# Kernel optimization log

Hardware: AMD Instinct MI355X
Metric: run time of the kernel (lower is better)

The kernel has to match this reference:

```python
import jax, jax.numpy as jnp
import numpy as np

B, N1, N2, D, O = 4, 256, 256, 64, 64
TEMP = 1.0
BN_EPS = 1e-5


def setup_inputs() -> dict:
    key = jax.random.key(0)
    ks = jax.random.split(key, 24)
    s = lambda n: 1.0 / np.sqrt(n)
    inp = {
        'x1': jax.random.normal(ks[0], (B, N1, D), jnp.float32),
        'x2': jax.random.normal(ks[1], (B, N2, D), jnp.float32),
        'W_t1': jax.random.normal(ks[2], (D, D), jnp.float32) * s(D),
        'b_t1': jnp.zeros((D,), jnp.float32),
        'W_t2': jax.random.normal(ks[3], (D, D), jnp.float32) * s(D),
        'b_t2': jnp.zeros((D,), jnp.float32),
        'W_att': jax.random.normal(ks[4], (D, O), jnp.float32) * s(D),
        'b_att': jnp.zeros((O,), jnp.float32),
        'W_attM': jax.random.normal(ks[5], (D, O), jnp.float32) * s(D),
        'b_attM': jnp.zeros((O,), jnp.float32),
        'w11': jax.random.normal(ks[6], (O, 1), jnp.float32) * s(O),
        'w22': jax.random.normal(ks[7], (O, 1), jnp.float32) * s(O),
        'w12': jax.random.normal(ks[8], (O, 1), jnp.float32) * s(O),
        'wM': jax.random.normal(ks[9], (O, 1), jnp.float32) * s(O),
        'W_pa': jax.random.normal(ks[10], (D, O), jnp.float32) * s(D),
        'b_pa': jnp.zeros((O,), jnp.float32),
        'W_po': jax.random.normal(ks[11], (D, O), jnp.float32) * s(D),
        'b_po': jnp.zeros((O,), jnp.float32),
        'W_paM': jax.random.normal(ks[12], (D, O), jnp.float32) * s(D),
        'b_paM': jnp.zeros((O,), jnp.float32),
        'W_poM': jax.random.normal(ks[13], (D, O), jnp.float32) * s(D),
        'b_poM': jnp.zeros((O,), jnp.float32),
        'gamma': jnp.ones((O,), jnp.float32),
        'beta': jnp.zeros((O,), jnp.float32),
    }
    return inp


def _forward(x1, x2, W_t1, b_t1, W_t2, b_t2, W_att, b_att, W_attM, b_attM,
             w11, w22, w12, wM, W_pa, b_pa, W_po, b_po, W_paM, b_paM,
             W_poM, b_poM, gamma, beta):
    n1 = x1.shape[1]
    h1 = x1 @ W_t1 + b_t1                      # (B,n1,D)
    h2 = x2 @ W_t2 + b_t2                      # (B,n2,D)
    x = jnp.concatenate([h1, h2], axis=1)      # (B,N,D)
    master = jnp.mean(x, axis=1, keepdims=True)  # (B,1,D)

    # --- type-blocked attention map ---
    pair = x[:, :, None, :] * x[:, None, :, :]          # (B,N,N,D)
    e = jnp.tanh(pair @ W_att + b_att)                   # (B,N,N,O)
    s11 = jnp.einsum('bijd,d->bij', e[:, :n1, :n1], w11[:, 0])
    s12 = jnp.einsum('bijd,d->bij', e[:, :n1, n1:], w12[:, 0])
    s21 = jnp.einsum('bijd,d->bij', e[:, n1:, :n1], w12[:, 0])
    s22 = jnp.einsum('bijd,d->bij', e[:, n1:, n1:], w22[:, 0])
    top = jnp.concatenate([s11, s12], axis=2)
    bot = jnp.concatenate([s21, s22], axis=2)
    scores = jnp.concatenate([top, bot], axis=1)         # (B,N,N)
    att = jax.nn.softmax(scores / TEMP, axis=2)          # softmax over source nodes (torch dim=-2 of (B,N,N,1))

    # --- master update ---
    m = jnp.tanh((x * master) @ W_attM + b_attM)         # (B,N,O)
    aM = jax.nn.softmax((m @ wM) / TEMP, axis=1)         # (B,N,1)
    agg_m = jnp.einsum('bn,bnd->bd', aM[:, :, 0], x)[:, None, :]  # (B,1,D)
    master_new = (agg_m @ W_paM + b_paM) + (master @ W_poM + b_poM)

    # --- node projection + BN(eval) + SELU ---
    agg = jnp.einsum('bij,bjd->bid', att, x)             # (B,N,D)
    y = (agg @ W_pa + b_pa) + (x @ W_po + b_po)          # (B,N,O)
    y = y / jnp.sqrt(1.0 + BN_EPS) * gamma + beta        # BN eval: mean=0, var=1
    y = jax.nn.selu(y)
    return y[:, :n1], y[:, n1:], master_new


def reference(x1, x2, W_t1, b_t1, W_t2, b_t2, W_att, b_att, W_attM, b_attM,
              w11, w22, w12, wM, W_pa, b_pa, W_po, b_po, W_paM, b_paM,
              W_poM, b_poM, gamma, beta):
    return _forward(x1, x2, W_t1, b_t1, W_t2, b_t2, W_att, b_att, W_attM,
                    b_attM, w11, w22, w12, wM, W_pa, b_pa, W_po, b_po,
                    W_paM, b_paM, W_poM, b_poM, gamma, beta)
```

## Files before the change

### kernel.cpp

```cpp
#include <hip/hip_runtime.h>

#define BB 4
#define NN 512
#define NH 256
#define DD 64

typedef __attribute__((ext_vector_type(8))) short bf16x8;
typedef __attribute__((ext_vector_type(16))) float f32x16;
union BF8 { bf16x8 v; unsigned int u[4]; };
union BF8Q { bf16x8 v; uint4 q; };

__device__ __forceinline__ float wred_sum(float v) {
  v += __shfl_xor(v, 32);
  v += __shfl_xor(v, 16);
  v += __shfl_xor(v, 8);
  v += __shfl_xor(v, 4);
  v += __shfl_xor(v, 2);
  v += __shfl_xor(v, 1);
  return v;
}

__device__ __forceinline__ float wred_max(float v) {
  v = fmaxf(v, __shfl_xor(v, 32));
  v = fmaxf(v, __shfl_xor(v, 16));
  v = fmaxf(v, __shfl_xor(v, 8));
  v = fmaxf(v, __shfl_xor(v, 4));
  v = fmaxf(v, __shfl_xor(v, 2));
  v = fmaxf(v, __shfl_xor(v, 1));
  return v;
}

__device__ __forceinline__ unsigned int cvtpk_bf16(float lo, float hi) {
  unsigned int r;
  asm("v_cvt_pk_bf16_f32 %0, %1, %2" : "=v"(r) : "v"(lo), "v"(hi));
  return r;
}

__device__ __forceinline__ float fast_exp2(float x) {
  float r;
  asm("v_exp_f32 %0, %1" : "=v"(r) : "v"(x));
  return r;
}

__device__ __forceinline__ float fast_tanh(float t) {
  t = fminf(15.f, fmaxf(-15.f, t));
  float z = __expf(2.f * t);
  return 1.f - 2.f * __builtin_amdgcn_rcpf(z + 1.f);
}

__device__ __forceinline__ float bflo(unsigned int u) { return __uint_as_float(u << 16); }
__device__ __forceinline__ float bfhi(unsigned int u) { return __uint_as_float(u & 0xffff0000u); }

__global__ __launch_bounds__(256)
void k1_build_x(const float* __restrict__ x1, const float* __restrict__ x2,
                const float* __restrict__ W_t1, const float* __restrict__ b_t1,
                const float* __restrict__ W_t2, const float* __restrict__ b_t2,
                unsigned int* __restrict__ XbfG) {
  const int tid = threadIdx.x;
  const int lane = tid & 63;
  const int rq = tid >> 6;
  const int r = blockIdx.x * 4 + rq;
  const int b = r >> 9;
  const int n = r & 511;
  const float* src; const float* W; const float* bias;
  if (n < NH) { src = x1 + (b * NH + n) * DD;        W = W_t1; bias = b_t1; }
  else        { src = x2 + (b * NH + (n - NH)) * DD; W = W_t2; bias = b_t2; }
  const float4* s4 = reinterpret_cast<const float4*>(src);
  float t0 = 0.f, t1 = 0.f, t2 = 0.f, t3 = 0.f;
#pragma unroll
  for (int c = 0; c < 16; ++c) {
    const float4 v = s4[c];
    t0 = fmaf(v.x, W[(4 * c + 0) * DD + lane], t0);
    t1 = fmaf(v.y, W[(4 * c + 1) * DD + lane], t1);
    t2 = fmaf(v.z, W[(4 * c + 2) * DD + lane], t2);
    t3 = fmaf(v.w, W[(4 * c + 3) * DD + lane], t3);
  }
  const float yv = ((t0 + t1) + (t2 + t3)) + bias[lane];
  const float nb = __shfl_down(yv, 1);
  if ((lane & 1) == 0) XbfG[r * 32 + (lane >> 1)] = cvtpk_bf16(yv, nb);
}

__global__ __launch_bounds__(512, 1)
void k_sc(const unsigned int* __restrict__ Xbf,
          const float* __restrict__ W_att, const float* __restrict__ b_att,
          const float* __restrict__ w11, const float* __restrict__ w22,
          const float* __restrict__ w12,
          float* __restrict__ scG) {
  const int b = blockIdx.y;
  const int bx = blockIdx.x;
  const int tid = threadIdx.x;
  const int lane = tid & 63;
  const int w = tid >> 6;
  const int l31 = lane & 31;
  const int half = lane >> 5;

  __shared__ __align__(16) float tblB[64];
  __shared__ __align__(16) unsigned int A2L[4][32];

  const unsigned int* __restrict__ Xb = Xbf + b * NN * 32;
  float* __restrict__ scb = scG + b * NN * NN;
  const float K2E = 2.8853900817779268f;

  if (tid < 64) {
    const int ot = tid >> 5, hf = (tid >> 4) & 1, r = tid & 15;
    const int o = ot * 32 + (r & 3) + 8 * (r >> 2) + 4 * hf;
    tblB[tid] = K2E * b_att[o];
  }
  if (tid >= 64 && tid < 320) {
    const int tt = tid - 64;
    const int comb = tt >> 6;
    const int idx = tt & 63;
    if (idx < 32) {
      const int ot = (idx >> 4) & 1, kg = (idx >> 3) & 1, hf = (idx >> 2) & 1, pp = idx & 3;
      const int it_ = comb >> 1, jt_ = comb & 1;
      const float* wsl = it_ ? (jt_ ? w22 : w12) : (jt_ ? w12 : w11);
      const int e0 = 2 * pp, e1 = 2 * pp + 1;
      const int o0 = ot * 32 + kg * 16 + (e0 & 3) + 8 * (e0 >> 2) + 4 * hf;
      const int o1 = ot * 32 + kg * 16 + (e1 & 3) + 8 * (e1 >> 2) + 4 * hf;
      A2L[comb][idx] = cvtpk_bf16(wsl[o0], wsl[o1]);
    }
  }

  BF8 Wp[2][4];
#pragma unroll
  for (int ot = 0; ot < 2; ++ot)
#pragma unroll
    for (int kt = 0; kt < 4; ++kt) {
      const int o = ot * 32 + l31;
#pragma unroll
      for (int pp = 0; pp < 4; ++pp) {
        const int d0 = kt * 16 + half * 8 + 2 * pp;
        Wp[ot][kt].u[pp] = cvtpk_bf16(W_att[d0 * DD + o], W_att[(d0 + 1) * DD + o]);
      }
    }

  __syncthreads();

  const int cminA = bx >> 4;
  const int n32A = 16 - cminA;
  const int rB = 510 - 2 * bx;
  const int cminB = (255 - bx) >> 4;
  const int njobs = 2 * (n32A + (16 - cminB));

#pragma unroll 1
  for (int jb = w; jb < njobs; jb += 8) {
    int row, c32;
    if (jb < 2 * n32A) { row = 2 * bx + (jb & 1); c32 = cminA + (jb >> 1); }
    else { const int tp = jb - 2 * n32A; row = rB + (tp & 1); c32 = cminB + (tp >> 1); }
    const int j0 = c32 * 32;
    const int comb = ((row >= NH) ? 2 : 0) | ((j0 >= NH) ? 1 : 0);

    BF8 Bi[4];
#pragma unroll
    for (int kt = 0; kt < 4; ++kt) {
      const uint4 xi = *reinterpret_cast<const uint4*>(Xb + row * 32 + kt * 8 + half * 4);
      const uint4 xj = *reinterpret_cast<const uint4*>(Xb + (j0 + l31) * 32 + kt * 8 + half * 4);
      Bi[kt].u[0] = cvtpk_bf16(bflo(xi.x) * bflo(xj.x), bfhi(xi.x) * bfhi(xj.x));
      Bi[kt].u[1] = cvtpk_bf16(bflo(xi.y) * bflo(xj.y), bfhi(xi.y) * bfhi(xj.y));
      Bi[kt].u[2] = cvtpk_bf16(bflo(xi.z) * bflo(xj.z), bfhi(xi.z) * bfhi(xj.z));
      Bi[kt].u[3] = cvtpk_bf16(bflo(xi.w) * bflo(xj.w), bfhi(xi.w) * bfhi(xj.w));
    }

    f32x16 C0 = {}, C1 = {};
#pragma unroll
    for (int kt = 0; kt < 4; ++kt) {
      C0 = __builtin_amdgcn_mfma_f32_32x32x16_bf16(Wp[0][kt].v, Bi[kt].v, C0, 0, 0, 0);
      C1 = __builtin_amdgcn_mfma_f32_32x32x16_bf16(Wp[1][kt].v, Bi[kt].v, C1, 0, 0, 0);
    }

    f32x16 D2 = {};
    const int base = half * 16;
#pragma unroll
    for (int ot = 0; ot < 2; ++ot) {
      float tv[16];
#pragma unroll
      for (int r = 0; r < 16; ++r) {
        const float Cr = (ot == 0) ? C0[r] : C1[r];
        const float arg = fmaf(Cr, K2E, tblB[ot * 32 + base + r]);
        const float e = fast_exp2(arg);
        tv[r] = fmaf(-2.f, __builtin_amdgcn_rcpf(e + 1.f), 1.f);
      }
      BF8 B2a, B2b;
#pragma unroll
      for (int pp = 0; pp < 4; ++pp) {
        B2a.u[pp] = cvtpk_bf16(tv[2 * pp], tv[2 * pp + 1]);
        B2b.u[pp] = cvtpk_bf16(tv[8 + 2 * pp], tv[9 + 2 * pp]);
      }
      BF8Q A2a, A2b;
      A2a.q = *reinterpret_cast<const uint4*>(&A2L[comb][ot * 16 + half * 4]);
      A2b.q = *reinterpret_cast<const uint4*>(&A2L[comb][ot * 16 + 8 + half * 4]);
      D2 = __builtin_amdgcn_mfma_f32_32x32x16_bf16(A2a.v, B2a.v, D2, 0, 0, 0);
      D2 = __builtin_amdgcn_mfma_f32_32x32x16_bf16(A2b.v, B2b.v, D2, 0, 0, 0);
    }
    const float pout = D2[0];
    if (lane < 32) {
      const int j = j0 + l31;
      if (j >= row) {
        scb[row * NN + j] = pout;
        if (j > row) scb[j * NN + row] = pout;
      }
    }
  }
}

__global__ __launch_bounds__(1024, 4)
void k_rest(const unsigned int* __restrict__ Xbf, const float* __restrict__ scG,
            const float* __restrict__ W_attM, const float* __restrict__ b_attM,
            const float* __restrict__ wM,
            const float* __restrict__ W_pa, const float* __restrict__ b_pa,
            const float* __restrict__ W_po, const float* __restrict__ b_po,
            const float* __restrict__ gamma, const float* __restrict__ beta,
            float* __restrict__ master, float* __restrict__ logits,
            float* __restrict__ out) {
  const int b = blockIdx.y;
  const int i0 = blockIdx.x * 8;
  const int tid = threadIdx.x;
  const int lane = tid & 63;
  const int w = tid >> 6;
  const int l31 = lane & 31;
  const int half = lane >> 5;

  __shared__ __align__(16) unsigned int XbfL[NN * 32];
  __shared__ __align__(16) float scL[8 * NN];
  __shared__ __align__(16) float red2[16][DD];
  __shared__ __align__(16) float aggP[32][DD];
  __shared__ __align__(16) float aggL[8][DD];
  __shared__ __align__(16) float mastL[64];

  const unsigned int* __restrict__ Xb = Xbf + b * NN * 32;

  {
#pragma unroll
    for (int k = 0; k < 4; ++k)
      reinterpret_cast<uint4*>(XbfL)[tid + k * 1024] =
          reinterpret_cast<const uint4*>(Xb)[tid + k * 1024];
  }
  {
    const int r8 = tid >> 7;
    const int c = (tid & 127) * 4;
    *reinterpret_cast<float4*>(&scL[r8 * NN + c]) =
        *reinterpret_cast<const float4*>(&scG[(b * NN + i0 + r8) * NN + c]);
  }
  __syncthreads();

  {
    float se = 0.f, so = 0.f;
    for (int r = w * 32; r < w * 32 + 32; ++r) {
      const unsigned int u = XbfL[r * 32 + l31];
      se += bflo(u); so += bfhi(u);
    }
    if (half == 0) {
      float2 pr; pr.x = se; pr.y = so;
      *reinterpret_cast<float2*>(&red2[w][l31 * 2]) = pr;
    }
  }
  __syncthreads();
  if (w == 0) {
    float s = 0.f;
#pragma unroll
    for (int k = 0; k < 16; ++k) s += red2[k][lane];
    s *= (1.f / 512.f);
    mastL[lane] = s;
    if (blockIdx.x == 0) master[b * DD + lane] = s;
  }

  const int row = w & 7, part = w >> 3;
  const int irow = i0 + row;
  float v[8];
#pragma unroll
  for (int k = 0; k < 8; ++k) v[k] = scL[row * NN + lane + 64 * k];
  __syncthreads();
  float mx = fmaxf(fmaxf(fmaxf(v[0], v[1]), fmaxf(v[2], v[3])),
                   fmaxf(fmaxf(v[4], v[5]), fmaxf(v[6], v[7])));
  mx = wred_max(mx);
  float ssum = 0.f;
#pragma unroll
  for (int k = 0; k < 8; ++k) { v[k] = __expf(v[k] - mx); ssum += v[k]; }
  ssum = wred_sum(ssum);
  const float inv = __builtin_amdgcn_rcpf(ssum);
#pragma unroll
  for (int k = 0; k < 4; ++k) {
    const int kk = part * 4 + k;
    scL[row * NN + lane + 64 * kk] = v[kk] * inv;
  }

  {
    float ae = 0.f, ao = 0.f;
    const int jb = part * 256 + half * 128;
#pragma unroll 4
    for (int it = 0; it < 32; ++it) {
      const int j = jb + it * 4;
      const float4 at = *reinterpret_cast<const float4*>(&scL[row * NN + j]);
      const unsigned int u0 = XbfL[(j + 0) * 32 + l31];
      const unsigned int u1 = XbfL[(j + 1) * 32 + l31];
      const unsigned int u2 = XbfL[(j + 2) * 32 + l31];
      const unsigned int u3 = XbfL[(j + 3) * 32 + l31];
      ae = fmaf(at.x, bflo(u0), ae); ao = fmaf(at.x, bfhi(u0), ao);
      ae = fmaf(at.y, bflo(u1), ae); ao = fmaf(at.y, bfhi(u1), ao);
      ae = fmaf(at.z, bflo(u2), ae); ao = fmaf(at.z, bfhi(u2), ao);
      ae = fmaf(at.w, bflo(u3), ae); ao = fmaf(at.w, bfhi(u3), ao);
    }
    float2 pr; pr.x = ae; pr.y = ao;
    *reinterpret_cast<float2*>(&aggP[row * 4 + part * 2 + half][l31 * 2]) = pr;
  }
  __syncthreads();

  uint4 xr[8];
#pragma unroll
  for (int s = 0; s < 8; ++s)
    xr[s] = *reinterpret_cast<const uint4*>(&XbfL[irow * 32 + s * 4]);

  if (part == 0) {
    const float aggv = aggP[row * 4 + 0][lane] + aggP[row * 4 + 1][lane] +
                       aggP[row * 4 + 2][lane] + aggP[row * 4 + 3][lane];
    aggL[row][lane] = aggv;
    float y = b_pa[lane] + b_po[lane];
#pragma unroll
    for (int s = 0; s < 8; ++s) {
      const float xd[8] = {bflo(xr[s].x), bfhi(xr[s].x), bflo(xr[s].y), bfhi(xr[s].y),
                           bflo(xr[s].z), bfhi(xr[s].z), bflo(xr[s].w), bfhi(xr[s].w)};
      const float4 agA = *reinterpret_cast<const float4*>(&aggL[row][s * 8]);
      const float4 agB = *reinterpret_cast<const float4*>(&aggL[row][s * 8 + 4]);
      const float ad[8] = {agA.x, agA.y, agA.z, agA.w, agB.x, agB.y, agB.z, agB.w};
#pragma unroll
      for (int q = 0; q < 8; ++q) {
        const int d = s * 8 + q;
        y = fmaf(ad[q], W_pa[d * DD + lane], y);
        y = fmaf(xd[q], W_po[d * DD + lane], y);
      }
    }
    const float RSQ = 0.9999950000374997f;
    y = y * RSQ * gamma[lane] + beta[lane];
    const float SC_ = 1.0507009873554805f;
    const float AL = 1.6732632423543772f;
    y = (y > 0.f) ? (SC_ * y) : (SC_ * AL * (__expf(y) - 1.f));
    const int off = (irow < NH) ? ((b * NH + irow) * DD + lane)
                                : (BB * NH * DD + (b * NH + (irow - NH)) * DD + lane);
    out[off] = y;
  } else {
    float lg = b_attM[lane];
#pragma unroll
    for (int s = 0; s < 8; ++s) {
      const float xd[8] = {bflo(xr[s].x), bfhi(xr[s].x), bflo(xr[s].y), bfhi(xr[s].y),
                           bflo(xr[s].z), bfhi(xr[s].z), bflo(xr[s].w), bfhi(xr[s].w)};
      const float4 mA = *reinterpret_cast<const float4*>(&mastL[s * 8]);
      const float4 mB = *reinterpret_cast<const float4*>(&mastL[s * 8 + 4]);
      const float md[8] = {mA.x, mA.y, mA.z, mA.w, mB.x, mB.y, mB.z, mB.w};
#pragma unroll
      for (int q = 0; q < 8; ++q) {
        const int d = s * 8 + q;
        lg = fmaf(xd[q] * md[q], W_attM[d * DD + lane], lg);
      }
    }
    const float th = fast_tanh(lg);
    const float s = wred_sum(th * wM[lane]);
    if (lane == 0) logits[b * NN + irow] = s;
  }
}

__global__ __launch_bounds__(256)
void k4_master_new(const unsigned int* __restrict__ Xbf, const float* __restrict__ master,
                   const float* __restrict__ logits,
                   const float* __restrict__ W_paM, const float* __restrict__ b_paM,
                   const float* __restrict__ W_poM, const float* __restrict__ b_poM,
                   float* __restrict__ out) {
  const int b = blockIdx.x;
  const int tid = threadIdx.x;
  const int lane = tid & 63;
  const int q = tid >> 6;
  const int l31 = lane & 31;
  const int half = lane >> 5;
  __shared__ float red[4][DD];
  __shared__ float r4[4];
  __shared__ float aggm_s[DD];
  __shared__ float mrow_s[DD];
  const float* lg = logits + b * NN;
  const float v0 = lg[tid];
  const float v1 = lg[tid + 256];
  float mx = wred_max(fmaxf(v0, v1));
  if (lane == 0) r4[q] = mx;
  __syncthreads();
  mx = fmaxf(fmaxf(r4[0], r4[1]), fmaxf(r4[2], r4[3]));
  float es = __expf(v0 - mx) + __expf(v1 - mx);
  es = wred_sum(es);
  __syncthreads();
  if (lane == 0) r4[q] = es;
  __syncthreads();
  const float S = r4[0] + r4[1] + r4[2] + r4[3];
  const float invS = 1.f / S;

  {
    float ae = 0.f, ao = 0.f;
    const int r0 = q * 128 + half * 64;
    for (int r = r0; r < r0 + 64; ++r) {
      const float a = __expf(lg[r] - mx);
      const unsigned int u = Xbf[b * NN * 32 + r * 32 + l31];
      ae = fmaf(a, bflo(u), ae);
      ao = fmaf(a, bfhi(u), ao);
    }
    ae += __shfl_xor(ae, 32);
    ao += __shfl_xor(ao, 32);
    if (half == 0) {
      float2 pr; pr.x = ae; pr.y = ao;
      *reinterpret_cast<float2*>(&red[q][l31 * 2]) = pr;
    }
  }
  __syncthreads();
  if (q == 0) {
    aggm_s[lane] =
        (red[0][lane] + red[1][lane] + red[2][lane] + red[3][lane]) * invS;
    mrow_s[lane] = master[b * DD + lane];
  }
  __syncthreads();
  float p = 0.f;
  for (int d = q * 16; d < q * 16 + 16; ++d) {
    p = fmaf(aggm_s[d], W_paM[d * DD + lane], p);
    p = fmaf(mrow_s[d], W_poM[d * DD + lane], p);
  }
  __syncthreads();
  red[q][lane] = p;
  __syncthreads();
  if (q == 0) {
    out[2 * BB * NH * DD + b * DD + lane] =
        red[0][lane] + red[1][lane] + red[2][lane] + red[3][lane] +
        b_paM[lane] + b_poM[lane];
  }
}

extern "C" void kernel_launch(void* const* d_in, const int* in_sizes, int n_in,
                              void* d_out, int out_size, void* d_ws, size_t ws_size,
                              hipStream_t stream) {
  const float* x1    = (const float*)d_in[0];
  const float* x2    = (const float*)d_in[1];
  const float* W_t1  = (const float*)d_in[2];
  const float* b_t1  = (const float*)d_in[3];
  const float* W_t2  = (const float*)d_in[4];
  const float* b_t2  = (const float*)d_in[5];
  const float* W_att = (const float*)d_in[6];
  const float* b_att = (const float*)d_in[7];
  const float* W_attM = (const float*)d_in[8];
  const float* b_attM = (const float*)d_in[9];
  const float* w11   = (const float*)d_in[10];
  const float* w22   = (const float*)d_in[11];
  const float* w12   = (const float*)d_in[12];
  const float* wM    = (const float*)d_in[13];
  const float* W_pa  = (const float*)d_in[14];
  const float* b_pa  = (const float*)d_in[15];
  const float* W_po  = (const float*)d_in[16];
  const float* b_po  = (const float*)d_in[17];
  const float* W_paM = (const float*)d_in[18];
  const float* b_paM = (const float*)d_in[19];
  const float* W_poM = (const float*)d_in[20];
  const float* b_poM = (const float*)d_in[21];
  const float* gamma = (const float*)d_in[22];
  const float* beta  = (const float*)d_in[23];

  float* ws     = (float*)d_ws;
  float* master = ws + 131072;
  float* logits = ws + 131328;
  float* scG    = ws + 133376;
  unsigned int* Xbf = (unsigned int*)(ws + 133376 + 1048576);
  float* out    = (float*)d_out;

  k1_build_x<<<512, 256, 0, stream>>>(x1, x2, W_t1, b_t1, W_t2, b_t2, Xbf);
  k_sc<<<dim3(128, 4), 512, 0, stream>>>(Xbf, W_att, b_att, w11, w22, w12, scG);
  k_rest<<<dim3(64, 4), 1024, 0, stream>>>(Xbf, scG, W_attM, b_attM, wM,
                                           W_pa, b_pa, W_po, b_po, gamma, beta,
                                           master, logits, out);
  k4_master_new<<<4, 256, 0, stream>>>(Xbf, master, logits, W_paM, b_paM, W_poM, b_poM, out);
}
```

Baseline: 50.33 us.

## Fuse master-node update into k_rest via last-block atomic counter

Removes the separate k4_master_new launch. The final block per batch to finish k_rest, detected through an atomic counter and threadfence, now does the master softmax, aggregation and projection using the X and master data already held in LDS. This saves one kernel launch and its global reloads. In exchange it adds fence and atomic overhead to every block and serialises the tail work on one block per batch. It also adds an unused fp32 X store in k1.

New measurement: 118.4 us. 2.35x slower.

```diff
diff --git a/kernel.cpp b/kernel.cpp
--- a/kernel.cpp
+++ b/kernel.cpp
@@ -55,8 +55,10 @@
 void k1_build_x(const float* __restrict__ x1, const float* __restrict__ x2,
                 const float* __restrict__ W_t1, const float* __restrict__ b_t1,
                 const float* __restrict__ W_t2, const float* __restrict__ b_t2,
-                unsigned int* __restrict__ XbfG) {
+                float* __restrict__ X, unsigned int* __restrict__ XbfG,
+                unsigned int* __restrict__ cnt) {
   const int tid = threadIdx.x;
+  if (blockIdx.x == 0 && tid < BB) cnt[tid] = 0u;
   const int lane = tid & 63;
   const int rq = tid >> 6;
   const int r = blockIdx.x * 4 + rq;
@@ -76,6 +78,7 @@
     t3 = fmaf(v.w, W[(4 * c + 3) * DD + lane], t3);
   }
   const float yv = ((t0 + t1) + (t2 + t3)) + bias[lane];
+  X[r * DD + lane] = yv;
   const float nb = __shfl_down(yv, 1);
   if ((lane & 1) == 0) XbfG[r * 32 + (lane >> 1)] = cvtpk_bf16(yv, nb);
 }
@@ -209,8 +212,11 @@
             const float* __restrict__ wM,
             const float* __restrict__ W_pa, const float* __restrict__ b_pa,
             const float* __restrict__ W_po, const float* __restrict__ b_po,
+            const float* __restrict__ W_paM, const float* __restrict__ b_paM,
+            const float* __restrict__ W_poM, const float* __restrict__ b_poM,
             const float* __restrict__ gamma, const float* __restrict__ beta,
             float* __restrict__ master, float* __restrict__ logits,
+            unsigned int* __restrict__ cnt,
             float* __restrict__ out) {
   const int b = blockIdx.y;
   const int i0 = blockIdx.x * 8;
@@ -226,6 +232,7 @@
   __shared__ __align__(16) float aggP[32][DD];
   __shared__ __align__(16) float aggL[8][DD];
   __shared__ __align__(16) float mastL[64];
+  __shared__ int isLast;
 
   const unsigned int* __restrict__ Xb = Xbf + b * NN * 32;
 
@@ -356,45 +363,46 @@
     const float s = wred_sum(th * wM[lane]);
     if (lane == 0) logits[b * NN + irow] = s;
   }
-}
-
-__global__ __launch_bounds__(256)
-void k4_master_new(const unsigned int* __restrict__ Xbf, const float* __restrict__ master,
-                   const float* __restrict__ logits,
-                   const float* __restrict__ W_paM, const float* __restrict__ b_paM,
-                   const float* __restrict__ W_poM, const float* __restrict__ b_poM,
-                   float* __restrict__ out) {
-  const int b = blockIdx.x;
-  const int tid = threadIdx.x;
-  const int lane = tid & 63;
-  const int q = tid >> 6;
-  const int l31 = lane & 31;
-  const int half = lane >> 5;
-  __shared__ float red[4][DD];
-  __shared__ float r4[4];
-  __shared__ float aggm_s[DD];
-  __shared__ float mrow_s[DD];
-  const float* lg = logits + b * NN;
-  const float v0 = lg[tid];
-  const float v1 = lg[tid + 256];
-  float mx = wred_max(fmaxf(v0, v1));
-  if (lane == 0) r4[q] = mx;
-  __syncthreads();
-  mx = fmaxf(fmaxf(r4[0], r4[1]), fmaxf(r4[2], r4[3]));
-  float es = __expf(v0 - mx) + __expf(v1 - mx);
-  es = wred_sum(es);
-  __syncthreads();
-  if (lane == 0) r4[q] = es;
-  __syncthreads();
-  const float S = r4[0] + r4[1] + r4[2] + r4[3];
+
+  __threadfence();
+  __syncthreads();
+  if (tid == 0) {
+    const unsigned int old = atomicAdd(&cnt[b], 1u);
+    isLast = (old == 63u) ? 1 : 0;
+  }
+  __syncthreads();
+  if (!isLast) return;
+  __threadfence();
+
+  if (tid < NN) scL[tid] = logits[b * NN + tid];
+  __syncthreads();
+
+  if (w < 8) {
+    const float vv = scL[w * 64 + lane];
+    const float m8 = wred_max(vv);
+    if (lane == 0) red2[0][w] = m8;
+  }
+  __syncthreads();
+  float dm = red2[0][0];
+#pragma unroll
+  for (int k = 1; k < 8; ++k) dm = fmaxf(dm, red2[0][k]);
+  if (w < 8) {
+    const float vv = scL[w * 64 + lane];
+    const float e8 = wred_sum(__expf(vv - dm));
+    if (lane == 0) red2[1][w] = e8;
+  }
+  __syncthreads();
+  float S = red2[1][0];
+#pragma unroll
+  for (int k = 1; k < 8; ++k) S += red2[1][k];
   const float invS = 1.f / S;
 
   {
     float ae = 0.f, ao = 0.f;
-    const int r0 = q * 128 + half * 64;
-    for (int r = r0; r < r0 + 64; ++r) {
-      const float a = __expf(lg[r] - mx);
-      const unsigned int u = Xbf[b * NN * 32 + r * 32 + l31];
+    const int r0 = w * 32 + half * 16;
+    for (int r = r0; r < r0 + 16; ++r) {
+      const float a = __expf(scL[r] - dm);
+      const unsigned int u = XbfL[r * 32 + l31];
       ae = fmaf(a, bflo(u), ae);
       ao = fmaf(a, bfhi(u), ao);
     }
@@ -402,28 +410,34 @@
     ao += __shfl_xor(ao, 32);
     if (half == 0) {
       float2 pr; pr.x = ae; pr.y = ao;
-      *reinterpret_cast<float2*>(&red[q][l31 * 2]) = pr;
-    }
-  }
-  __syncthreads();
-  if (q == 0) {
-    aggm_s[lane] =
-        (red[0][lane] + red[1][lane] + red[2][lane] + red[3][lane]) * invS;
-    mrow_s[lane] = master[b * DD + lane];
-  }
-  __syncthreads();
-  float p = 0.f;
-  for (int d = q * 16; d < q * 16 + 16; ++d) {
-    p = fmaf(aggm_s[d], W_paM[d * DD + lane], p);
-    p = fmaf(mrow_s[d], W_poM[d * DD + lane], p);
-  }
-  __syncthreads();
-  red[q][lane] = p;
-  __syncthreads();
-  if (q == 0) {
-    out[2 * BB * NH * DD + b * DD + lane] =
-        red[0][lane] + red[1][lane] + red[2][lane] + red[3][lane] +
-        b_paM[lane] + b_poM[lane];
+      *reinterpret_cast<float2*>(&aggP[w][l31 * 2]) = pr;
+    }
+  }
+  __syncthreads();
+  if (w == 0) {
+    float s = 0.f;
+#pragma unroll
+    for (int k = 0; k < 16; ++k) s += aggP[k][lane];
+    aggL[0][lane] = s * invS;
+  }
+  __syncthreads();
+
+  {
+    float p = 0.f;
+#pragma unroll
+    for (int k = 0; k < 4; ++k) {
+      const int d = w * 4 + k;
+      p = fmaf(aggL[0][d], W_paM[d * DD + lane], p);
+      p = fmaf(mastL[d],  W_poM[d * DD + lane], p);
+    }
+    red2[w][lane] = p;
+  }
+  __syncthreads();
+  if (w == 0) {
+    float s = 0.f;
+#pragma unroll
+    for (int k = 0; k < 16; ++k) s += red2[k][lane];
+    out[2 * BB * NH * DD + b * DD + lane] = s + b_paM[lane] + b_poM[lane];
   }
 }
 
@@ -456,16 +470,18 @@
   const float* beta  = (const float*)d_in[23];
 
   float* ws     = (float*)d_ws;
+  float* X      = ws;
   float* master = ws + 131072;
   float* logits = ws + 131328;
   float* scG    = ws + 133376;
   unsigned int* Xbf = (unsigned int*)(ws + 133376 + 1048576);
+  unsigned int* cnt = Xbf + 65536;
   float* out    = (float*)d_out;
 
-  k1_build_x<<<512, 256, 0, stream>>>(x1, x2, W_t1, b_t1, W_t2, b_t2, Xbf);
+  k1_build_x<<<512, 256, 0, stream>>>(x1, x2, W_t1, b_t1, W_t2, b_t2, X, Xbf, cnt);
   k_sc<<<dim3(128, 4), 512, 0, stream>>>(Xbf, W_att, b_att, w11, w22, w12, scG);
   k_rest<<<dim3(64, 4), 1024, 0, stream>>>(Xbf, scG, W_attM, b_attM, wM,
-                                           W_pa, b_pa, W_po, b_po, gamma, beta,
-                                           master, logits, out);
-  k4_master_new<<<4, 256, 0, stream>>>(Xbf, master, logits, W_paM, b_paM, W_poM, b_poM, out);
-}
+                                           W_pa, b_pa, W_po, b_po,
+                                           W_paM, b_paM, W_poM, b_poM,
+                                           gamma, beta, master, logits, cnt, out);
+}
```
